# Optimization experiments

Measured on AMD Instinct MI355X. Metric: run time of the kernel, lower is better.

## Reference

```python
import jax, jax.numpy as jnp
import numpy as np

B, S, E = 8, 2048, 512

def setup_inputs() -> dict:
    key = jax.random.key(0)
    ks = jax.random.split(key, 7)
    Q = jax.random.normal(ks[0], (B, S, E), dtype=jnp.float32)
    K = jax.random.normal(ks[1], (B, S, E), dtype=jnp.float32)
    pad_mask = jax.random.randint(ks[2], (B, S, S), 0, 2).astype(bool)
    # torch nn.Linear weights are [out, in]; y = x @ W.T + b
    sc = 1.0 / np.sqrt(E)
    Wq = jax.random.uniform(ks[3], (E, E), jnp.float32, -sc, sc)
    Wk = jax.random.uniform(ks[4], (E, E), jnp.float32, -sc, sc)
    Wv = jax.random.uniform(ks[5], (E, E), jnp.float32, -sc, sc)
    Wp = jax.random.uniform(ks[6], (E, E), jnp.float32, -sc, sc)
    bp = jnp.zeros((E,), jnp.float32)
    return {"Q": Q, "K": K, "pad_mask": pad_mask, "Wq": Wq, "Wk": Wk, "Wv": Wv, "Wp": Wp, "bp": bp}

def reference(Q, K, pad_mask, Wq, Wk, Wv, Wp, bp):
    scale = E ** (-0.5)
    V = K  # V aliases K before projection, as in the original
    q = jnp.einsum('bse,fe->bsf', Q, Wq)   # q_map (no bias)
    k = jnp.einsum('bse,fe->bsf', K, Wk)   # k_map
    v = jnp.einsum('bse,fe->bsf', V, Wv)   # v_map
    scores = jnp.einsum('bqe,bke->bqk', q, k) * scale  # [B,S,S]
    scores = jnp.where(pad_mask, -1e9, scores)
    attn = jax.nn.softmax(scores, axis=-1)
    out = jnp.einsum('bqk,bke->bqe', attn, v)
    out = jnp.einsum('bse,fe->bsf', out, Wp) + bp       # proj
    return q + out  # residual uses projected Q (faithful to source)
```

## Files before the change

kernel.cpp:

```cpp
#include <hip/hip_runtime.h>
#include <hip/hip_bf16.h>

typedef short v8s __attribute__((ext_vector_type(8)));
typedef float v4f __attribute__((ext_vector_type(4)));

static constexpr int BB = 8;
static constexpr int SS = 2048;
static constexpr int EE = 512;

enum { EPI_T = 0, EPI_SCALE_T = 1, EPI_FINAL_T = 2 };

struct EpiParams {
  float scale;
  const float* bias;
  const __hip_bfloat16* resid;
  int resid_ld;
  int trans_ld;
};

__global__ __launch_bounds__(256) void cast_f32_bf16(const float* __restrict__ x,
                                                     __hip_bfloat16* __restrict__ y, int n) {
  int i = (blockIdx.x * 256 + threadIdx.x) * 8;
  if (i >= n) return;
  float4 f0 = ((const float4*)(x + i))[0];
  float4 f1 = ((const float4*)(x + i))[1];
  alignas(16) __hip_bfloat16 h[8];
  h[0] = __float2bfloat16(f0.x); h[1] = __float2bfloat16(f0.y);
  h[2] = __float2bfloat16(f0.z); h[3] = __float2bfloat16(f0.w);
  h[4] = __float2bfloat16(f1.x); h[5] = __float2bfloat16(f1.y);
  h[6] = __float2bfloat16(f1.z); h[7] = __float2bfloat16(f1.w);
  *(uint4*)(y + i) = *(uint4*)h;
}

__device__ __forceinline__ void stage_tile64(const __hip_bfloat16* __restrict__ G,
                                             int row0, int ld, int k0,
                                             __hip_bfloat16* lds, int wave, int lane) {
#pragma unroll
  for (int t = 0; t < 4; ++t) {
    const int p = (wave * 4 + t) * 64 + lane;
    const int row = p >> 3;
    const int gp = p & 7;
    const int g = gp ^ (row & 7);
    const __hip_bfloat16* src = G + (unsigned long long)(row0 + row) * ld + k0 + g * 8;
    __builtin_amdgcn_global_load_lds(
        (const __attribute__((address_space(1))) void*)src,
        (__attribute__((address_space(3))) void*)(lds + (wave * 4 + t) * 512),
        16, 0, 0);
  }
}

template <int EPI>
__global__ __launch_bounds__(256, 2) void gemm_bt(
    const __hip_bfloat16* __restrict__ Ag, const __hip_bfloat16* __restrict__ Bg,
    void* __restrict__ Cg, int M, int N, int K, int lda, int ldb,
    unsigned long long strideAz, unsigned long long strideBz, unsigned long long strideCz,
    EpiParams ep) {
  __shared__ __hip_bfloat16 As[128 * 64];
  __shared__ __hip_bfloat16 Bs[128 * 64];

  const int tid = threadIdx.x;
  const int lane = tid & 63;
  const int wave = tid >> 6;
  const int wr = wave >> 1;
  const int wc = wave & 1;
  const int z = blockIdx.z;
  const int m0 = blockIdx.y * 128;
  const int n0 = blockIdx.x * 128;

  Ag += (unsigned long long)z * strideAz;
  Bg += (unsigned long long)z * strideBz;

  v4f acc[4][4];
  const v4f vzero = {0.f, 0.f, 0.f, 0.f};
#pragma unroll
  for (int i = 0; i < 4; ++i)
#pragma unroll
    for (int j = 0; j < 4; ++j) acc[i][j] = vzero;

  const int fr = lane & 15;
  const int fq = lane >> 4;

  for (int k0 = 0; k0 < K; k0 += 64) {
    __syncthreads();
    stage_tile64(Ag, m0, lda, k0, As, wave, lane);
    stage_tile64(Bg, n0, ldb, k0, Bs, wave, lane);
    __syncthreads();

#pragma unroll
    for (int ks = 0; ks < 2; ++ks) {
      const int gq = ks * 4 + fq;
      v8s a[4], b[4];
#pragma unroll
      for (int i = 0; i < 4; ++i) {
        const int r = wr * 64 + i * 16 + fr;
        a[i] = *(const v8s*)&As[r * 64 + ((gq ^ (r & 7)) * 8)];
      }
#pragma unroll
      for (int j = 0; j < 4; ++j) {
        const int r = wc * 64 + j * 16 + fr;
        b[j] = *(const v8s*)&Bs[r * 64 + ((gq ^ (r & 7)) * 8)];
      }
#pragma unroll
      for (int i = 0; i < 4; ++i)
#pragma unroll
        for (int j = 0; j < 4; ++j)
          acc[i][j] = __builtin_amdgcn_mfma_f32_16x16x32_bf16(a[i], b[j], acc[i][j], 0, 0, 0);
    }
  }

  const int cf = lane & 15;
  const int rq = (lane >> 4) * 4;
  const int colBase = n0 + wc * 64;
  const int rowBase = m0 + wr * 64;

#pragma unroll
  for (int i = 0; i < 4; ++i) {
    const int row0 = rowBase + i * 16 + rq;
    float4 b4;
    if constexpr (EPI == EPI_FINAL_T) b4 = *(const float4*)&ep.bias[row0];
#pragma unroll
    for (int j = 0; j < 4; ++j) {
      const int col = colBase + j * 16 + cf;
      if constexpr (EPI == EPI_T) {
        __hip_bfloat16* C = (__hip_bfloat16*)Cg + (unsigned long long)z * strideCz;
        alignas(8) __hip_bfloat16 t4[4];
#pragma unroll
        for (int r = 0; r < 4; ++r) t4[r] = __float2bfloat16(acc[i][j][r]);
        *(ushort4*)&C[(unsigned long long)col * ep.trans_ld + row0] = *(ushort4*)t4;
      } else if constexpr (EPI == EPI_SCALE_T) {
        __hip_bfloat16* C = (__hip_bfloat16*)Cg + (unsigned long long)z * strideCz;
        alignas(8) __hip_bfloat16 t4[4];
#pragma unroll
        for (int r = 0; r < 4; ++r) t4[r] = __float2bfloat16(acc[i][j][r] * ep.scale);
        *(ushort4*)&C[(unsigned long long)col * ep.trans_ld + row0] = *(ushort4*)t4;
      } else {
        float* C = (float*)Cg + (unsigned long long)z * strideCz;
        ushort4 r4 = *(const ushort4*)&ep.resid[(unsigned long long)col * ep.resid_ld + row0];
        float4 o;
        o.x = acc[i][j][0] + b4.x + __bfloat162float(*(__hip_bfloat16*)&r4.x);
        o.y = acc[i][j][1] + b4.y + __bfloat162float(*(__hip_bfloat16*)&r4.y);
        o.z = acc[i][j][2] + b4.z + __bfloat162float(*(__hip_bfloat16*)&r4.z);
        o.w = acc[i][j][3] + b4.w + __bfloat162float(*(__hip_bfloat16*)&r4.w);
        *(float4*)&C[(unsigned long long)col * ep.trans_ld + row0] = o;
      }
    }
  }
}

__global__ __launch_bounds__(256) void softmax_rows(__hip_bfloat16* __restrict__ sc,
                                                    const unsigned char* __restrict__ mask) {
  const unsigned long long row = blockIdx.x;
  __hip_bfloat16* p = sc + row * (unsigned long long)SS;
  const int tid = threadIdx.x;
  const int lane = tid & 63;
  const int wv = tid >> 6;

  alignas(16) __hip_bfloat16 hv[8];
  ((uint4*)hv)[0] = *(const uint4*)&p[tid * 8];
  const unsigned long long mbits =
      *(const unsigned long long*)(mask + row * (unsigned long long)SS + tid * 8);

  float v[8];
  float m = -3.4e38f;
#pragma unroll
  for (int i = 0; i < 8; ++i) {
    v[i] = ((mbits >> (8 * i)) & 0xffull) ? -1e9f : __bfloat162float(hv[i]);
    m = fmaxf(m, v[i]);
  }
#pragma unroll
  for (int off = 32; off >= 1; off >>= 1) m = fmaxf(m, __shfl_xor(m, off));

  __shared__ float redm[4];
  __shared__ float reds[4];
  if (lane == 0) redm[wv] = m;
  __syncthreads();
  m = fmaxf(fmaxf(redm[0], redm[1]), fmaxf(redm[2], redm[3]));

  float s = 0.f;
#pragma unroll
  for (int i = 0; i < 8; ++i) {
    v[i] = __expf(v[i] - m);
    s += v[i];
  }
#pragma unroll
  for (int off = 32; off >= 1; off >>= 1) s += __shfl_xor(s, off);
  if (lane == 0) reds[wv] = s;
  __syncthreads();
  s = reds[0] + reds[1] + reds[2] + reds[3];
  const float inv = 1.0f / s;

#pragma unroll
  for (int i = 0; i < 8; ++i) hv[i] = __float2bfloat16(v[i] * inv);
  *(uint4*)&p[tid * 8] = ((uint4*)hv)[0];
}

extern "C" void kernel_launch(void* const* d_in, const int* in_sizes, int n_in,
                              void* d_out, int out_size, void* d_ws, size_t ws_size,
                              hipStream_t stream) {
  const float* Q = (const float*)d_in[0];
  const float* K = (const float*)d_in[1];
  const unsigned char* mask = (const unsigned char*)d_in[2];
  const float* Wq = (const float*)d_in[3];
  const float* Wk = (const float*)d_in[4];
  const float* Wv = (const float*)d_in[5];
  const float* Wp = (const float*)d_in[6];
  const float* bp = (const float*)d_in[7];
  float* out = (float*)d_out;

  char* ws = (char*)d_ws;
  const unsigned long long MB = 1024ull * 1024ull;
  __hip_bfloat16* qb = (__hip_bfloat16*)(ws + 0 * MB);
  __hip_bfloat16* kb = (__hip_bfloat16*)(ws + 16 * MB);
  __hip_bfloat16* ob = kb;
  __hip_bfloat16* vT = (__hip_bfloat16*)(ws + 32 * MB);
  __hip_bfloat16* Wqb = (__hip_bfloat16*)(ws + 48 * MB);
  __hip_bfloat16* Wkb = Wqb + 512 * 512;
  __hip_bfloat16* Wvb = Wkb + 512 * 512;
  __hip_bfloat16* Wpb = Wvb + 512 * 512;
  __hip_bfloat16* sc = (__hip_bfloat16*)(ws + 64 * MB);
  __hip_bfloat16* Qc = sc;
  __hip_bfloat16* Kc = sc + 8ull * MB;

  dim3 blk(256, 1, 1);
  const int nQK = BB * SS * EE;
  const int nW = EE * EE;

  cast_f32_bf16<<<dim3(nQK / 2048, 1, 1), blk, 0, stream>>>(Q, Qc, nQK);
  cast_f32_bf16<<<dim3(nQK / 2048, 1, 1), blk, 0, stream>>>(K, Kc, nQK);
  cast_f32_bf16<<<dim3(nW / 2048, 1, 1), blk, 0, stream>>>(Wq, Wqb, nW);
  cast_f32_bf16<<<dim3(nW / 2048, 1, 1), blk, 0, stream>>>(Wk, Wkb, nW);
  cast_f32_bf16<<<dim3(nW / 2048, 1, 1), blk, 0, stream>>>(Wv, Wvb, nW);
  cast_f32_bf16<<<dim3(nW / 2048, 1, 1), blk, 0, stream>>>(Wp, Wpb, nW);

  EpiParams epq{};
  epq.trans_ld = EE;
  gemm_bt<EPI_T><<<dim3((BB * SS) / 128, EE / 128, 1), blk, 0, stream>>>(
      Wqb, Qc, qb, EE, BB * SS, EE, EE, EE, 0ull, 0ull, 0ull, epq);

  gemm_bt<EPI_T><<<dim3((BB * SS) / 128, EE / 128, 1), blk, 0, stream>>>(
      Wkb, Kc, kb, EE, BB * SS, EE, EE, EE, 0ull, 0ull, 0ull, epq);

  EpiParams epv{};
  epv.trans_ld = BB * SS;
  gemm_bt<EPI_T><<<dim3(EE / 128, (BB * SS) / 128, 1), blk, 0, stream>>>(
      Kc, Wvb, vT, BB * SS, EE, EE, EE, EE, 0ull, 0ull, 0ull, epv);

  EpiParams eps{};
  eps.scale = 0.044194173824159216f;
  eps.trans_ld = SS;
  gemm_bt<EPI_SCALE_T><<<dim3(SS / 128, SS / 128, BB), blk, 0, stream>>>(
      kb, qb, sc, SS, SS, EE, EE, EE,
      (unsigned long long)SS * EE, (unsigned long long)SS * EE,
      (unsigned long long)SS * SS, eps);

  softmax_rows<<<dim3(BB * SS, 1, 1), blk, 0, stream>>>(sc, mask);

  EpiParams epo{};
  epo.trans_ld = EE;
  gemm_bt<EPI_T><<<dim3(SS / 128, EE / 128, BB), blk, 0, stream>>>(
      vT, sc, ob, EE, SS, SS, BB * SS, SS,
      (unsigned long long)SS, (unsigned long long)SS * SS,
      (unsigned long long)SS * EE, epo);

  EpiParams epf{};
  epf.bias = bp;
  epf.resid = qb;
  epf.resid_ld = EE;
  epf.trans_ld = EE;
  gemm_bt<EPI_FINAL_T><<<dim3((BB * SS) / 128, EE / 128, 1), blk, 0, stream>>>(
      Wpb, ob, out, EE, BB * SS, EE, EE, EE, 0ull, 0ull, 0ull, epf);
}
```

Before: 408.3 us.

## Stage GEMM epilogues through LDS for coalesced stores and batch cast/QKV launches

The GEMM epilogue used to write transposed 8-byte fragments scattered by column. It now stages the accumulator tile in LDS and writes full coalesced 16-byte rows, with operands swapped so outputs come out untransposed. The six cast kernels become one multi-segment launch, and the Q/K/V projections become one gridded launch. Occupancy hints rise to 3 blocks per CU. In exchange, the epilogue adds extra LDS traffic and barriers.

```diff
diff --git a/kernel.cpp b/kernel.cpp
--- a/kernel.cpp
+++ b/kernel.cpp
@@ -4,24 +4,31 @@
 typedef short v8s __attribute__((ext_vector_type(8)));
 typedef float v4f __attribute__((ext_vector_type(4)));
 
-static constexpr int BB = 8;
-static constexpr int SS = 2048;
-static constexpr int EE = 512;
-
-enum { EPI_T = 0, EPI_SCALE_T = 1, EPI_FINAL_T = 2 };
+static constexpr int BB = 8, SS = 2048, EE = 512;
+
+enum { EPI_BF16 = 0, EPI_SCALE = 1, EPI_FINAL = 2 };
 
 struct EpiParams {
   float scale;
   const float* bias;
   const __hip_bfloat16* resid;
   int resid_ld;
-  int trans_ld;
 };
 
-__global__ __launch_bounds__(256) void cast_f32_bf16(const float* __restrict__ x,
-                                                     __hip_bfloat16* __restrict__ y, int n) {
-  int i = (blockIdx.x * 256 + threadIdx.x) * 8;
-  if (i >= n) return;
+static constexpr int SMEM_BYTES = 34816;
+
+struct CastParams {
+  const float* src[6];
+  __hip_bfloat16* dst[6];
+  int nblk[6];
+};
+
+__global__ __launch_bounds__(256) void cast_multi(CastParams cp) {
+  int b = blockIdx.x, seg = 0, base = 0;
+  while (b - base >= cp.nblk[seg]) { base += cp.nblk[seg]; ++seg; }
+  const float* x = cp.src[seg] + (unsigned long long)(b - base) * 2048;
+  __hip_bfloat16* y = cp.dst[seg] + (unsigned long long)(b - base) * 2048;
+  int i = threadIdx.x * 8;
   float4 f0 = ((const float4*)(x + i))[0];
   float4 f1 = ((const float4*)(x + i))[1];
   alignas(16) __hip_bfloat16 h[8];
@@ -39,8 +46,7 @@
   for (int t = 0; t < 4; ++t) {
     const int p = (wave * 4 + t) * 64 + lane;
     const int row = p >> 3;
-    const int gp = p & 7;
-    const int g = gp ^ (row & 7);
+    const int g = (p & 7) ^ (row & 7);
     const __hip_bfloat16* src = G + (unsigned long long)(row0 + row) * ld + k0 + g * 8;
     __builtin_amdgcn_global_load_lds(
         (const __attribute__((address_space(1))) void*)src,
@@ -50,25 +56,18 @@
 }
 
 template <int EPI>
-__global__ __launch_bounds__(256, 2) void gemm_bt(
-    const __hip_bfloat16* __restrict__ Ag, const __hip_bfloat16* __restrict__ Bg,
-    void* __restrict__ Cg, int M, int N, int K, int lda, int ldb,
-    unsigned long long strideAz, unsigned long long strideBz, unsigned long long strideCz,
-    EpiParams ep) {
-  __shared__ __hip_bfloat16 As[128 * 64];
-  __shared__ __hip_bfloat16 Bs[128 * 64];
+__device__ __forceinline__ void gemm_body(const __hip_bfloat16* Ag, const __hip_bfloat16* Bg,
+                                          void* Cg, int K, int lda, int ldb, int ldc,
+                                          int m0, int n0, const EpiParams& ep,
+                                          unsigned char* smem) {
+  __hip_bfloat16* As = (__hip_bfloat16*)smem;
+  __hip_bfloat16* Bs = As + 128 * 64;
 
   const int tid = threadIdx.x;
   const int lane = tid & 63;
   const int wave = tid >> 6;
   const int wr = wave >> 1;
   const int wc = wave & 1;
-  const int z = blockIdx.z;
-  const int m0 = blockIdx.y * 128;
-  const int n0 = blockIdx.x * 128;
-
-  Ag += (unsigned long long)z * strideAz;
-  Bg += (unsigned long long)z * strideBz;
 
   v4f acc[4][4];
   const v4f vzero = {0.f, 0.f, 0.f, 0.f};
@@ -110,41 +109,105 @@
 
   const int cf = lane & 15;
   const int rq = (lane >> 4) * 4;
-  const int colBase = n0 + wc * 64;
-  const int rowBase = m0 + wr * 64;
-
-#pragma unroll
-  for (int i = 0; i < 4; ++i) {
-    const int row0 = rowBase + i * 16 + rq;
-    float4 b4;
-    if constexpr (EPI == EPI_FINAL_T) b4 = *(const float4*)&ep.bias[row0];
-#pragma unroll
-    for (int j = 0; j < 4; ++j) {
-      const int col = colBase + j * 16 + cf;
-      if constexpr (EPI == EPI_T) {
-        __hip_bfloat16* C = (__hip_bfloat16*)Cg + (unsigned long long)z * strideCz;
-        alignas(8) __hip_bfloat16 t4[4];
-#pragma unroll
-        for (int r = 0; r < 4; ++r) t4[r] = __float2bfloat16(acc[i][j][r]);
-        *(ushort4*)&C[(unsigned long long)col * ep.trans_ld + row0] = *(ushort4*)t4;
-      } else if constexpr (EPI == EPI_SCALE_T) {
-        __hip_bfloat16* C = (__hip_bfloat16*)Cg + (unsigned long long)z * strideCz;
-        alignas(8) __hip_bfloat16 t4[4];
-#pragma unroll
-        for (int r = 0; r < 4; ++r) t4[r] = __float2bfloat16(acc[i][j][r] * ep.scale);
-        *(ushort4*)&C[(unsigned long long)col * ep.trans_ld + row0] = *(ushort4*)t4;
-      } else {
-        float* C = (float*)Cg + (unsigned long long)z * strideCz;
-        ushort4 r4 = *(const ushort4*)&ep.resid[(unsigned long long)col * ep.resid_ld + row0];
-        float4 o;
-        o.x = acc[i][j][0] + b4.x + __bfloat162float(*(__hip_bfloat16*)&r4.x);
-        o.y = acc[i][j][1] + b4.y + __bfloat162float(*(__hip_bfloat16*)&r4.y);
-        o.z = acc[i][j][2] + b4.z + __bfloat162float(*(__hip_bfloat16*)&r4.z);
-        o.w = acc[i][j][3] + b4.w + __bfloat162float(*(__hip_bfloat16*)&r4.w);
-        *(float4*)&C[(unsigned long long)col * ep.trans_ld + row0] = o;
+
+  __syncthreads();
+
+  if constexpr (EPI != EPI_FINAL) {
+    __hip_bfloat16* Ct = (__hip_bfloat16*)smem;
+    const int ST = 136;
+#pragma unroll
+    for (int i = 0; i < 4; ++i) {
+      const int rl = wr * 64 + i * 16 + rq;
+#pragma unroll
+      for (int j = 0; j < 4; ++j) {
+        const int col = wc * 64 + j * 16 + cf;
+#pragma unroll
+        for (int r = 0; r < 4; ++r) {
+          float v = acc[i][j][r];
+          if constexpr (EPI == EPI_SCALE) v *= ep.scale;
+          Ct[(rl + r) * ST + col] = __float2bfloat16(v);
+        }
       }
     }
-  }
+    __syncthreads();
+    __hip_bfloat16* C = (__hip_bfloat16*)Cg;
+#pragma unroll
+    for (int c = 0; c < 8; ++c) {
+      const int idx = c * 256 + tid;
+      const int row = idx >> 4;
+      const int colc = (idx & 15) * 8;
+      *(v8s*)&C[(unsigned long long)(m0 + row) * ldc + n0 + colc] =
+          *(const v8s*)&Ct[row * ST + colc];
+    }
+  } else {
+    float* Cf = (float*)smem;
+    const int ST = 132;
+    float* C = (float*)Cg;
+#pragma unroll
+    for (int h = 0; h < 2; ++h) {
+      if (wr == h) {
+#pragma unroll
+        for (int i = 0; i < 4; ++i) {
+          const int rl = i * 16 + rq;
+#pragma unroll
+          for (int j = 0; j < 4; ++j) {
+            const int col = wc * 64 + j * 16 + cf;
+#pragma unroll
+            for (int r = 0; r < 4; ++r) Cf[(rl + r) * ST + col] = acc[i][j][r];
+          }
+        }
+      }
+      __syncthreads();
+#pragma unroll
+      for (int c = 0; c < 8; ++c) {
+        const int idx = c * 256 + tid;
+        const int row = idx >> 5;
+        const int colc = (idx & 31) * 4;
+        const int grow = m0 + h * 64 + row;
+        const int gcol = n0 + colc;
+        float4 v = *(const float4*)&Cf[row * ST + colc];
+        float4 b4 = *(const float4*)&ep.bias[gcol];
+        ushort4 r4 = *(const ushort4*)&ep.resid[(unsigned long long)grow * ep.resid_ld + gcol];
+        v.x += b4.x + __bfloat162float(*(__hip_bfloat16*)&r4.x);
+        v.y += b4.y + __bfloat162float(*(__hip_bfloat16*)&r4.y);
+        v.z += b4.z + __bfloat162float(*(__hip_bfloat16*)&r4.z);
+        v.w += b4.w + __bfloat162float(*(__hip_bfloat16*)&r4.w);
+        *(float4*)&C[(unsigned long long)grow * ldc + gcol] = v;
+      }
+      if (h == 0) __syncthreads();
+    }
+  }
+}
+
+template <int EPI>
+__global__ __launch_bounds__(256, 3) void gemm_bt(
+    const __hip_bfloat16* __restrict__ Ag, const __hip_bfloat16* __restrict__ Bg,
+    void* __restrict__ Cg, int K, int lda, int ldb, int ldc,
+    unsigned long long sAz, unsigned long long sBz, unsigned long long sCz, EpiParams ep) {
+  __shared__ __align__(16) unsigned char smem[SMEM_BYTES];
+  const unsigned long long z = blockIdx.z;
+  void* Cz;
+  if constexpr (EPI == EPI_FINAL) Cz = (void*)((float*)Cg + z * sCz);
+  else Cz = (void*)((__hip_bfloat16*)Cg + z * sCz);
+  gemm_body<EPI>(Ag + z * sAz, Bg + z * sBz, Cz, K, lda, ldb, ldc,
+                 blockIdx.y * 128, blockIdx.x * 128, ep, smem);
+}
+
+struct QKVParams {
+  const __hip_bfloat16* A[3];
+  const __hip_bfloat16* B[3];
+  __hip_bfloat16* C[3];
+  int ldc[3];
+};
+
+__global__ __launch_bounds__(256, 3) void gemm_qkv(QKVParams p) {
+  __shared__ __align__(16) unsigned char smem[SMEM_BYTES];
+  const int z = blockIdx.z;
+  const int bm = (z == 2) ? blockIdx.y : blockIdx.x;
+  const int bn = (z == 2) ? blockIdx.x : blockIdx.y;
+  EpiParams ep{};
+  gemm_body<EPI_BF16>(p.A[z], p.B[z], p.C[z], EE, EE, EE, p.ldc[z],
+                      bm * 128, bn * 128, ep, smem);
 }
 
 __global__ __launch_bounds__(256) void softmax_rows(__hip_bfloat16* __restrict__ sc,
@@ -225,48 +288,41 @@
   const int nQK = BB * SS * EE;
   const int nW = EE * EE;
 
-  cast_f32_bf16<<<dim3(nQK / 2048, 1, 1), blk, 0, stream>>>(Q, Qc, nQK);
-  cast_f32_bf16<<<dim3(nQK / 2048, 1, 1), blk, 0, stream>>>(K, Kc, nQK);
-  cast_f32_bf16<<<dim3(nW / 2048, 1, 1), blk, 0, stream>>>(Wq, Wqb, nW);
-  cast_f32_bf16<<<dim3(nW / 2048, 1, 1), blk, 0, stream>>>(Wk, Wkb, nW);
-  cast_f32_bf16<<<dim3(nW / 2048, 1, 1), blk, 0, stream>>>(Wv, Wvb, nW);
-  cast_f32_bf16<<<dim3(nW / 2048, 1, 1), blk, 0, stream>>>(Wp, Wpb, nW);
-
-  EpiParams epq{};
-  epq.trans_ld = EE;
-  gemm_bt<EPI_T><<<dim3((BB * SS) / 128, EE / 128, 1), blk, 0, stream>>>(
-      Wqb, Qc, qb, EE, BB * SS, EE, EE, EE, 0ull, 0ull, 0ull, epq);
-
-  gemm_bt<EPI_T><<<dim3((BB * SS) / 128, EE / 128, 1), blk, 0, stream>>>(
-      Wkb, Kc, kb, EE, BB * SS, EE, EE, EE, 0ull, 0ull, 0ull, epq);
-
-  EpiParams epv{};
-  epv.trans_ld = BB * SS;
-  gemm_bt<EPI_T><<<dim3(EE / 128, (BB * SS) / 128, 1), blk, 0, stream>>>(
-      Kc, Wvb, vT, BB * SS, EE, EE, EE, EE, 0ull, 0ull, 0ull, epv);
+  CastParams cp;
+  cp.src[0] = Q;  cp.dst[0] = Qc;  cp.nblk[0] = nQK / 2048;
+  cp.src[1] = K;  cp.dst[1] = Kc;  cp.nblk[1] = nQK / 2048;
+  cp.src[2] = Wq; cp.dst[2] = Wqb; cp.nblk[2] = nW / 2048;
+  cp.src[3] = Wk; cp.dst[3] = Wkb; cp.nblk[3] = nW / 2048;
+  cp.src[4] = Wv; cp.dst[4] = Wvb; cp.nblk[4] = nW / 2048;
+  cp.src[5] = Wp; cp.dst[5] = Wpb; cp.nblk[5] = nW / 2048;
+  int totalBlk = 2 * (nQK / 2048) + 4 * (nW / 2048);
+  cast_multi<<<dim3(totalBlk, 1, 1), blk, 0, stream>>>(cp);
+
+  QKVParams qp;
+  qp.A[0] = Qc;  qp.B[0] = Wqb; qp.C[0] = qb; qp.ldc[0] = EE;
+  qp.A[1] = Kc;  qp.B[1] = Wkb; qp.C[1] = kb; qp.ldc[1] = EE;
+  qp.A[2] = Wvb; qp.B[2] = Kc;  qp.C[2] = vT; qp.ldc[2] = BB * SS;
+  gemm_qkv<<<dim3((BB * SS) / 128, EE / 128, 3), blk, 0, stream>>>(qp);
 
   EpiParams eps{};
   eps.scale = 0.044194173824159216f;
-  eps.trans_ld = SS;
-  gemm_bt<EPI_SCALE_T><<<dim3(SS / 128, SS / 128, BB), blk, 0, stream>>>(
-      kb, qb, sc, SS, SS, EE, EE, EE,
+  gemm_bt<EPI_SCALE><<<dim3(SS / 128, SS / 128, BB), blk, 0, stream>>>(
+      qb, kb, sc, EE, EE, EE, SS,
       (unsigned long long)SS * EE, (unsigned long long)SS * EE,
       (unsigned long long)SS * SS, eps);
 
   softmax_rows<<<dim3(BB * SS, 1, 1), blk, 0, stream>>>(sc, mask);
 
-  EpiParams epo{};
-  epo.trans_ld = EE;
-  gemm_bt<EPI_T><<<dim3(SS / 128, EE / 128, BB), blk, 0, stream>>>(
-      vT, sc, ob, EE, SS, SS, BB * SS, SS,
-      (unsigned long long)SS, (unsigned long long)SS * SS,
-      (unsigned long long)SS * EE, epo);
+  EpiParams ep0{};
+  gemm_bt<EPI_BF16><<<dim3(EE / 128, SS / 128, BB), blk, 0, stream>>>(
+      sc, vT, ob, SS, SS, BB * SS, EE,
+      (unsigned long long)SS * SS, (unsigned long long)SS,
+      (unsigned long long)SS * EE, ep0);
 
   EpiParams epf{};
   epf.bias = bp;
   epf.resid = qb;
   epf.resid_ld = EE;
-  epf.trans_ld = EE;
-  gemm_bt<EPI_FINAL_T><<<dim3((BB * SS) / 128, EE / 128, 1), blk, 0, stream>>>(
-      Wpb, ob, out, EE, BB * SS, EE, EE, EE, 0ull, 0ull, 0ull, epf);
-}
+  gemm_bt<EPI_FINAL><<<dim3(EE / 128, (BB * SS) / 128, 1), blk, 0, stream>>>(
+      ob, Wpb, out, EE, EE, EE, EE, 0ull, 0ull, 0ull, epf);
+}
```

New measurement: 383.6 us. -6.1%, faster.
